# Kernel tuning notes

Hardware: AMD Instinct MI355X
Metric: run time of the kernel (lower is better)

## Reference

```python
import jax, jax.numpy as jnp
import numpy as np

B, S, H, O, K = 32, 2048, 768, 768, 64


def setup_inputs() -> dict:
    key = jax.random.key(0)
    k0, k1, k2, k3, k4 = jax.random.split(key, 5)
    hidden = jax.random.normal(k0, (B, S, H), dtype=jnp.float32)
    token_idxs = jnp.sort(jax.random.randint(k1, (B, K), 0, S), axis=1)
    subject_hidden = jax.random.normal(k2, (B, H), dtype=jnp.float32)
    Wa = jax.random.normal(k3, (2 * H, 1), dtype=jnp.float32) * 0.02
    ba = jnp.zeros((1,), dtype=jnp.float32)
    Wo = jax.random.normal(k4, (H, O), dtype=jnp.float32) * 0.02
    bo = jnp.zeros((O,), dtype=jnp.float32)
    return {"hidden": hidden, "token_idxs": token_idxs, "subject_hidden": subject_hidden,
            "Wa": Wa, "ba": ba, "Wo": Wo, "bo": bo}


def reference(hidden, token_idxs, subject_hidden, Wa, ba, Wo, bo):
    b, s, h = hidden.shape
    # binary token mask [B,S] from per-example index lists (duplicates collapse to 1)
    mask = jnp.zeros((b, s), hidden.dtype).at[jnp.arange(b)[:, None], token_idxs].set(1.0)
    m3 = mask[:, :, None]                                  # [B,S,1]
    masked = hidden * m3                                   # masked_hidden
    subj_rep = subject_hidden[:, None, :] * m3             # broadcast + mask, no repeat
    # alignment_model(concat(subj, masked)) done as split matmul to avoid [B,S,2H]
    scores = subj_rep @ Wa[:h] + masked @ Wa[h:] + ba      # [B,S,1]
    # masked softmax over the selected tokens only (dim=0 over selected entries == seq axis)
    logits = jnp.where(m3 > 0, scores, jnp.float32(-1e9))
    attention_weights = jax.nn.softmax(logits, axis=1) * m3  # exact zeros off-mask
    pooled = jnp.einsum("bsh,bs->bh", masked, attention_weights[:, :, 0])
    transformed = jnp.tanh(pooled @ Wo + bo)
    return transformed, attention_weights
```

## Files before the change

### kernel.cpp

```cpp
#include <hip/hip_runtime.h>
#include <cmath>

#define Bb 32
#define Ss 2048
#define Hh 768
#define Oo 768
#define Kk 64

__global__ __launch_bounds__(256) void scores_kernel(
    const float* __restrict__ hidden,
    const int*   __restrict__ idxs,
    const float* __restrict__ Wa,
    float* __restrict__ scores,
    float* __restrict__ aw_out)
{
    const int tid  = threadIdx.x;
    const int lane = tid & 63;
    const int wid  = blockIdx.x * 4 + (tid >> 6);
    const int gid  = blockIdx.x * 256 + tid;

    if (gid < (Bb * Ss / 4))
        ((float4*)aw_out)[gid] = make_float4(0.f, 0.f, 0.f, 0.f);

    const int b = wid >> 6;
    const int j = wid & 63;
    const int t_idx = idxs[b * Kk + j];

    const float4* row4 = (const float4*)(hidden + ((size_t)b * Ss + t_idx) * Hh);
    const float4* wa4  = (const float4*)(Wa + Hh);
    float p = 0.f;
    #pragma unroll
    for (int t = 0; t < 3; ++t) {
        const float4 r = row4[lane + 64 * t];
        const float4 w = wa4[lane + 64 * t];
        p += r.x * w.x + r.y * w.y + r.z * w.z + r.w * w.w;
    }
    #pragma unroll
    for (int m = 32; m >= 1; m >>= 1) p += __shfl_xor(p, m);
    if (lane == 0) scores[wid] = p;
}

__global__ __launch_bounds__(64) void softmax_kernel(
    const int*   __restrict__ idxs,
    const float* __restrict__ subj,
    const float* __restrict__ Wa,
    const float* __restrict__ ba,
    const float* __restrict__ scores,
    float* __restrict__ aw,
    float* __restrict__ aw_out)
{
    const int b = blockIdx.x;
    const int j = threadIdx.x;

    const float4* s4  = (const float4*)(subj + b * Hh);
    const float4* wa4 = (const float4*)Wa;
    float p = 0.f;
    #pragma unroll
    for (int t = 0; t < 3; ++t) {
        const float4 r = s4[j + 64 * t];
        const float4 w = wa4[j + 64 * t];
        p += r.x * w.x + r.y * w.y + r.z * w.z + r.w * w.w;
    }
    #pragma unroll
    for (int m = 32; m >= 1; m >>= 1) p += __shfl_xor(p, m);
    const float sconst = p + ba[0];

    const int  myidx   = idxs[b * Kk + j];
    const int  previdx = (j > 0) ? idxs[b * Kk + j - 1] : -1;
    const bool active  = (j == 0) || (myidx != previdx);

    float sc = active ? (scores[b * Kk + j] + sconst) : -3.0e38f;
    float mx = sc;
    #pragma unroll
    for (int m = 32; m >= 1; m >>= 1) mx = fmaxf(mx, __shfl_xor(mx, m));
    const float e = active ? expf(sc - mx) : 0.f;
    float sum = e;
    #pragma unroll
    for (int m = 32; m >= 1; m >>= 1) sum += __shfl_xor(sum, m);
    const float w = e / sum;

    aw[b * Kk + j] = w;
    if (active) aw_out[(size_t)b * Ss + myidx] = w;
}

__global__ __launch_bounds__(1024) void pool_gemm_kernel(
    const float* __restrict__ hidden,
    const int*   __restrict__ idxs,
    const float* __restrict__ aw,
    const float* __restrict__ Wo,
    const float* __restrict__ bo,
    float* __restrict__ out)
{
    const int b   = blockIdx.x / 3;
    const int oc  = blockIdx.x % 3;
    const int tid = threadIdx.x;

    __shared__ float s_aw[Kk];
    __shared__ int   s_idx[Kk];
    __shared__ float s_pool[Hh];
    __shared__ float s_part[4 * 256];

    if (tid < Kk) {
        s_aw[tid]  = aw[b * Kk + tid];
        s_idx[tid] = idxs[b * Kk + tid];
    }
    __syncthreads();

    if (tid < Hh) {
        float acc = 0.f;
        #pragma unroll 8
        for (int j = 0; j < Kk; ++j)
            acc += s_aw[j] * hidden[((size_t)b * Ss + s_idx[j]) * Hh + tid];
        s_pool[tid] = acc;
    }
    __syncthreads();

    const int ol = tid & 255;
    const int o  = oc * 256 + ol;
    const int hg = tid >> 8;
    const int h0 = hg * 192;
    float acc = 0.f;
    #pragma unroll 8
    for (int h = h0; h < h0 + 192; ++h)
        acc = fmaf(s_pool[h], Wo[h * Oo + o], acc);
    s_part[hg * 256 + ol] = acc;
    __syncthreads();

    if (tid < 256) {
        const int oo = oc * 256 + tid;
        const float s = s_part[tid] + s_part[256 + tid] + s_part[512 + tid]
                      + s_part[768 + tid] + bo[oo];
        out[b * Oo + oo] = tanhf(s);
    }
}

extern "C" void kernel_launch(void* const* d_in, const int* in_sizes, int n_in,
                              void* d_out, int out_size, void* d_ws, size_t ws_size,
                              hipStream_t stream) {
    const float* hidden = (const float*)d_in[0];
    const int*   idxs   = (const int*)d_in[1];
    const float* subj   = (const float*)d_in[2];
    const float* Wa     = (const float*)d_in[3];
    const float* ba     = (const float*)d_in[4];
    const float* Wo     = (const float*)d_in[5];
    const float* bo     = (const float*)d_in[6];

    float* out    = (float*)d_out;
    float* aw_out = out + Bb * Oo;
    float* scores = (float*)d_ws;
    float* aw     = scores + Bb * Kk;

    scores_kernel <<<512, 256, 0, stream>>>(hidden, idxs, Wa, scores, aw_out);
    softmax_kernel<<<Bb, 64, 0, stream>>>(idxs, subj, Wa, ba, scores, aw, aw_out);
    pool_gemm_kernel<<<Bb * 3, 1024, 0, stream>>>(hidden, idxs, aw, Wo, bo, out);
}
```

Measured before the change: 262.6 us.

## Fuse softmax into pooling and batch the output GEMM across examples

Softmax is merged into a pooling kernel split across three hidden-chunks per example, and the pooled vectors go to workspace. A separate GEMM kernel maps the 32 batch rows onto lanes so each Wo column is loaded once for all examples, instead of being re-streamed by every per-example block. This removes the repeated full reads of the output weight matrix but adds a workspace round trip for the pooled vectors. The GEMM grid is small (96 blocks), so it may not fill the device.

Result: slower. 282.4 us (+7.6%).

```diff
diff --git a/kernel.cpp b/kernel.cpp
--- a/kernel.cpp
+++ b/kernel.cpp
@@ -40,98 +40,89 @@
     if (lane == 0) scores[wid] = p;
 }
 
-__global__ __launch_bounds__(64) void softmax_kernel(
+__global__ __launch_bounds__(256) void softmax_pool_kernel(
+    const float* __restrict__ hidden,
     const int*   __restrict__ idxs,
     const float* __restrict__ subj,
     const float* __restrict__ Wa,
     const float* __restrict__ ba,
     const float* __restrict__ scores,
-    float* __restrict__ aw,
-    float* __restrict__ aw_out)
+    float* __restrict__ aw_out,
+    float* __restrict__ pooled)
 {
-    const int b = blockIdx.x;
-    const int j = threadIdx.x;
+    const int b   = blockIdx.x / 3;
+    const int hc  = blockIdx.x % 3;
+    const int tid = threadIdx.x;
 
-    const float4* s4  = (const float4*)(subj + b * Hh);
-    const float4* wa4 = (const float4*)Wa;
-    float p = 0.f;
-    #pragma unroll
-    for (int t = 0; t < 3; ++t) {
-        const float4 r = s4[j + 64 * t];
-        const float4 w = wa4[j + 64 * t];
-        p += r.x * w.x + r.y * w.y + r.z * w.z + r.w * w.w;
+    __shared__ float s_aw[Kk];
+    __shared__ int   s_idx[Kk];
+
+    if (tid < Kk) {
+        const int j     = tid;
+        const int myidx = idxs[b * Kk + j];
+        s_idx[j] = myidx;
+
+        const float4* s4  = (const float4*)(subj + b * Hh);
+        const float4* wa4 = (const float4*)Wa;
+        float p = 0.f;
+        #pragma unroll
+        for (int t = 0; t < 3; ++t) {
+            const float4 r = s4[j + 64 * t];
+            const float4 w = wa4[j + 64 * t];
+            p += r.x * w.x + r.y * w.y + r.z * w.z + r.w * w.w;
+        }
+        #pragma unroll
+        for (int m = 32; m >= 1; m >>= 1) p += __shfl_xor(p, m);
+        const float sconst = p + ba[0];
+
+        const int  previdx = __shfl_up(myidx, 1);
+        const bool active  = (j == 0) || (myidx != previdx);
+
+        float sc = active ? (scores[b * Kk + j] + sconst) : -3.0e38f;
+        float mx = sc;
+        #pragma unroll
+        for (int m = 32; m >= 1; m >>= 1) mx = fmaxf(mx, __shfl_xor(mx, m));
+        const float e = active ? expf(sc - mx) : 0.f;
+        float sum = e;
+        #pragma unroll
+        for (int m = 32; m >= 1; m >>= 1) sum += __shfl_xor(sum, m);
+        const float w = e / sum;
+
+        s_aw[j] = w;
+        if (hc == 0 && active) aw_out[(size_t)b * Ss + myidx] = w;
     }
-    #pragma unroll
-    for (int m = 32; m >= 1; m >>= 1) p += __shfl_xor(p, m);
-    const float sconst = p + ba[0];
+    __syncthreads();
 
-    const int  myidx   = idxs[b * Kk + j];
-    const int  previdx = (j > 0) ? idxs[b * Kk + j - 1] : -1;
-    const bool active  = (j == 0) || (myidx != previdx);
-
-    float sc = active ? (scores[b * Kk + j] + sconst) : -3.0e38f;
-    float mx = sc;
-    #pragma unroll
-    for (int m = 32; m >= 1; m >>= 1) mx = fmaxf(mx, __shfl_xor(mx, m));
-    const float e = active ? expf(sc - mx) : 0.f;
-    float sum = e;
-    #pragma unroll
-    for (int m = 32; m >= 1; m >>= 1) sum += __shfl_xor(sum, m);
-    const float w = e / sum;
-
-    aw[b * Kk + j] = w;
-    if (active) aw_out[(size_t)b * Ss + myidx] = w;
+    const int h = hc * 256 + tid;
+    float acc = 0.f;
+    #pragma unroll 8
+    for (int j = 0; j < Kk; ++j)
+        acc += s_aw[j] * hidden[((size_t)b * Ss + s_idx[j]) * Hh + h];
+    pooled[b * Hh + h] = acc;
 }
 
-__global__ __launch_bounds__(1024) void pool_gemm_kernel(
-    const float* __restrict__ hidden,
-    const int*   __restrict__ idxs,
-    const float* __restrict__ aw,
+__global__ __launch_bounds__(256) void gemm_tanh_kernel(
+    const float* __restrict__ pooled,
     const float* __restrict__ Wo,
     const float* __restrict__ bo,
     float* __restrict__ out)
 {
-    const int b   = blockIdx.x / 3;
-    const int oc  = blockIdx.x % 3;
-    const int tid = threadIdx.x;
+    const int bc = blockIdx.x;
+    const int b  = threadIdx.x & 31;
+    const int o  = bc * 8 + (threadIdx.x >> 5);
 
-    __shared__ float s_aw[Kk];
-    __shared__ int   s_idx[Kk];
-    __shared__ float s_pool[Hh];
-    __shared__ float s_part[4 * 256];
-
-    if (tid < Kk) {
-        s_aw[tid]  = aw[b * Kk + tid];
-        s_idx[tid] = idxs[b * Kk + tid];
+    const float4* p4 = (const float4*)(pooled + b * Hh);
+    float a0 = 0.f, a1 = 0.f, a2 = 0.f, a3 = 0.f;
+    #pragma unroll 4
+    for (int i = 0; i < Hh / 4; ++i) {
+        const float4 pv = p4[i];
+        const int h = 4 * i;
+        a0 = fmaf(pv.x, Wo[(h + 0) * Oo + o], a0);
+        a1 = fmaf(pv.y, Wo[(h + 1) * Oo + o], a1);
+        a2 = fmaf(pv.z, Wo[(h + 2) * Oo + o], a2);
+        a3 = fmaf(pv.w, Wo[(h + 3) * Oo + o], a3);
     }
-    __syncthreads();
-
-    if (tid < Hh) {
-        float acc = 0.f;
-        #pragma unroll 8
-        for (int j = 0; j < Kk; ++j)
-            acc += s_aw[j] * hidden[((size_t)b * Ss + s_idx[j]) * Hh + tid];
-        s_pool[tid] = acc;
-    }
-    __syncthreads();
-
-    const int ol = tid & 255;
-    const int o  = oc * 256 + ol;
-    const int hg = tid >> 8;
-    const int h0 = hg * 192;
-    float acc = 0.f;
-    #pragma unroll 8
-    for (int h = h0; h < h0 + 192; ++h)
-        acc = fmaf(s_pool[h], Wo[h * Oo + o], acc);
-    s_part[hg * 256 + ol] = acc;
-    __syncthreads();
-
-    if (tid < 256) {
-        const int oo = oc * 256 + tid;
-        const float s = s_part[tid] + s_part[256 + tid] + s_part[512 + tid]
-                      + s_part[768 + tid] + bo[oo];
-        out[b * Oo + oo] = tanhf(s);
-    }
+    out[b * Oo + o] = tanhf(a0 + a1 + a2 + a3 + bo[o]);
 }
 
 extern "C" void kernel_launch(void* const* d_in, const int* in_sizes, int n_in,
@@ -148,9 +139,10 @@
     float* out    = (float*)d_out;
     float* aw_out = out + Bb * Oo;
     float* scores = (float*)d_ws;
-    float* aw     = scores + Bb * Kk;
+    float* pooled = scores + Bb * Kk;
 
-    scores_kernel <<<512, 256, 0, stream>>>(hidden, idxs, Wa, scores, aw_out);
-    softmax_kernel<<<Bb, 64, 0, stream>>>(idxs, subj, Wa, ba, scores, aw, aw_out);
-    pool_gemm_kernel<<<Bb * 3, 1024, 0, stream>>>(hidden, idxs, aw, Wo, bo, out);
+    scores_kernel      <<<512, 256, 0, stream>>>(hidden, idxs, Wa, scores, aw_out);
+    softmax_pool_kernel<<<Bb * 3, 256, 0, stream>>>(hidden, idxs, subj, Wa, ba,
+                                                    scores, aw_out, pooled);
+    gemm_tanh_kernel   <<<96, 256, 0, stream>>>(pooled, Wo, bo, out);
 }
```
